# Kernel optimization log

Measured on AMD Instinct MI355X. Metric: run time of the kernel, lower is better.

## Reference

```python
import jax, jax.numpy as jnp
import numpy as np

H = W = 224  # output confidence map size


def setup_inputs() -> dict:
    key = jax.random.key(0)
    k_x, k_w1, k_b1, k_w2, k_b2 = jax.random.split(key, 5)
    N = 500_000  # number of detections in the clip
    x = jax.random.uniform(k_x, (N, 7), dtype=jnp.float32)
    W1 = jax.random.normal(k_w1, (7, 64), dtype=jnp.float32) * (1.0 / np.sqrt(7.0))
    b1 = jax.random.normal(k_b1, (64,), dtype=jnp.float32) * 0.01
    W2 = jax.random.normal(k_w2, (64, H * W), dtype=jnp.float32) * (1.0 / 8.0)
    b2 = jax.random.normal(k_b2, (H * W,), dtype=jnp.float32) * 0.01
    return {"x": x, "W1": W1, "b1": b1, "W2": W2, "b2": b2}


def reference(x, W1, b1, W2, b2):
    # Encoder branch of Track_Block.forward:
    # silu -> Linear(7,64) -> silu -> mean over detections -> Linear(64,224*224)
    # -> silu -> reshape(224,224) -> clamp(0,1)
    h = jax.nn.silu(x)                       # [N, 7]
    h = jax.nn.silu(h @ W1 + b1)             # [N, 64]
    m = jnp.mean(h, axis=0)                  # [64] (mean over detection dim)
    e = jax.nn.silu(m @ W2 + b2)             # [50176]
    return jnp.clip(e.reshape(H, W), 0.0, 1.0)
```

## Files before the change

kernel.cpp:

```cpp
#include <hip/hip_runtime.h>
#include <hip/hip_bf16.h>

#define HWOUT 50176
#define NBLK  1024
#define CHUNK 256

typedef __attribute__((ext_vector_type(8))) short short8;
typedef __attribute__((ext_vector_type(4))) float f32x4;

__device__ __forceinline__ float fast_sigmoid(float x) {
    float t = __builtin_amdgcn_exp2f(-1.44269504088896340736f * x);
    return __builtin_amdgcn_rcpf(1.0f + t);
}
__device__ __forceinline__ float silu_f(float x) { return x * fast_sigmoid(x); }

__device__ __forceinline__ short to_bf16_bits(float f) {
    unsigned u = __builtin_bit_cast(unsigned, f);
    u += 0x7FFFu + ((u >> 16) & 1u);
    return (short)(u >> 16);
}

__global__ __launch_bounds__(256) void k_stage1(const float* __restrict__ x,
                                                const float* __restrict__ W1,
                                                const float* __restrict__ b1,
                                                float* __restrict__ partial,
                                                int N) {
    __shared__ short xs[CHUNK * 8];
    __shared__ float red[4][64];
    const int t = threadIdx.x;
    const int lane = t & 63;
    const int wave = t >> 6;

    const int krow = (lane >> 4) * 8;
    const int c = lane & 15;
    short8 bf[4];
    float bcol[4];
#pragma unroll
    for (int g = 0; g < 4; ++g) {
#pragma unroll
        for (int j = 0; j < 8; ++j) {
            int k = krow + j;
            float v = (k < 7) ? W1[k * 64 + g * 16 + c] : 0.0f;
            bf[g][j] = to_bf16_bits(v);
        }
        bcol[g] = b1[g * 16 + c];
    }

    float accf[4] = {0.0f, 0.0f, 0.0f, 0.0f};
    const int nchunk = (N + CHUNK - 1) / CHUNK;
    const short8 zero8 = {0, 0, 0, 0, 0, 0, 0, 0};
    const f32x4 zero4 = {0.0f, 0.0f, 0.0f, 0.0f};

    for (int ch = blockIdx.x; ch < nchunk; ch += NBLK) {
        const int row = ch * CHUNK + t;
        __syncthreads();
        {
            float v[7];
            if (row < N) {
#pragma unroll
                for (int k = 0; k < 7; ++k) v[k] = x[row * 7 + k];
            } else {
#pragma unroll
                for (int k = 0; k < 7; ++k) v[k] = 0.0f;
            }
            short8 p;
#pragma unroll
            for (int k = 0; k < 7; ++k) p[k] = to_bf16_bits(silu_f(v[k]));
            p[7] = 0;
            *reinterpret_cast<short8*>(&xs[t * 8]) = p;
        }
        __syncthreads();

        const bool full = (ch * CHUNK + CHUNK <= N);
        const int chbase = ch * CHUNK;
#pragma unroll
        for (int tt = 0; tt < 4; ++tt) {
            const int tile = wave * 4 + tt;
            short8 av = *reinterpret_cast<short8*>(&xs[(tile * 16 + c) * 8]);
            av = (lane < 16) ? av : zero8;
#pragma unroll
            for (int g = 0; g < 4; ++g) {
                f32x4 d = __builtin_amdgcn_mfma_f32_16x16x32_bf16(av, bf[g], zero4, 0, 0, 0);
                if (full) {
#pragma unroll
                    for (int r = 0; r < 4; ++r) accf[g] += silu_f(d[r] + bcol[g]);
                } else {
                    const int r0 = chbase + tile * 16 + (lane >> 4) * 4;
#pragma unroll
                    for (int r = 0; r < 4; ++r) {
                        float s = silu_f(d[r] + bcol[g]);
                        accf[g] += (r0 + r < N) ? s : 0.0f;
                    }
                }
            }
        }
    }

#pragma unroll
    for (int g = 0; g < 4; ++g) {
        accf[g] += __shfl_xor(accf[g], 16, 64);
        accf[g] += __shfl_xor(accf[g], 32, 64);
    }
    if (lane < 16) {
#pragma unroll
        for (int g = 0; g < 4; ++g) red[wave][g * 16 + lane] = accf[g];
    }
    __syncthreads();
    if (t < 64)
        partial[blockIdx.x * 64 + t] = red[0][t] + red[1][t] + red[2][t] + red[3][t];
}

__global__ __launch_bounds__(256) void k_out2(const float* __restrict__ partial,
                                              const float* __restrict__ W2,
                                              const float* __restrict__ b2,
                                              float* __restrict__ out,
                                              float invN) {
    __shared__ float4 red[256];
    __shared__ float ml[64];
    const int t = threadIdx.x;
    const int c4 = t & 15;
    const int grp = t >> 4;
    const float4* p4 = reinterpret_cast<const float4*>(partial);

    float4 s = {0.0f, 0.0f, 0.0f, 0.0f};
#pragma unroll 8
    for (int r = grp; r < NBLK; r += 16) {
        float4 v = p4[r * 16 + c4];
        s.x += v.x; s.y += v.y; s.z += v.z; s.w += v.w;
    }
    red[t] = s;
    __syncthreads();
    if (t < 16) {
        float4 a = {0.0f, 0.0f, 0.0f, 0.0f};
#pragma unroll
        for (int g = 0; g < 16; ++g) {
            float4 v = red[g * 16 + t];
            a.x += v.x; a.y += v.y; a.z += v.z; a.w += v.w;
        }
        ml[4 * t + 0] = a.x * invN;
        ml[4 * t + 1] = a.y * invN;
        ml[4 * t + 2] = a.z * invN;
        ml[4 * t + 3] = a.w * invN;
    }
    __syncthreads();

    const int j = blockIdx.x * 256 + t;
    float acc = b2[j];
#pragma unroll
    for (int k4 = 0; k4 < 16; ++k4) {
        float4 mv = *reinterpret_cast<float4*>(&ml[k4 * 4]);
        acc = fmaf(mv.x, W2[(k4 * 4 + 0) * HWOUT + j], acc);
        acc = fmaf(mv.y, W2[(k4 * 4 + 1) * HWOUT + j], acc);
        acc = fmaf(mv.z, W2[(k4 * 4 + 2) * HWOUT + j], acc);
        acc = fmaf(mv.w, W2[(k4 * 4 + 3) * HWOUT + j], acc);
    }
    float e = silu_f(acc);
    out[j] = fminf(fmaxf(e, 0.0f), 1.0f);
}

extern "C" void kernel_launch(void* const* d_in, const int* in_sizes, int n_in,
                              void* d_out, int out_size, void* d_ws, size_t ws_size,
                              hipStream_t stream) {
    const float* x  = (const float*)d_in[0];
    const float* W1 = (const float*)d_in[1];
    const float* b1 = (const float*)d_in[2];
    const float* W2 = (const float*)d_in[3];
    const float* b2 = (const float*)d_in[4];
    float* out = (float*)d_out;

    const int N = in_sizes[0] / 7;
    float* partial = (float*)d_ws;

    k_stage1<<<NBLK, 256, 0, stream>>>(x, W1, b1, partial, N);
    k_out2<<<HWOUT / 256, 256, 0, stream>>>(partial, W2, b2, out, 1.0f / (float)N);
}
```

Before: 25.74 us.

## Fuse both stages into one persistent kernel with atomic grid barrier

Merges the MLP-mean stage and the output projection into a single kernel of 256 blocks of 1024 threads. After each block writes its partial sums, an atomic counter with a spin-wait acts as a grid-wide barrier, and every block then reduces all partials itself. Each block computes 196 outputs, splitting K across four thread groups. Rows are loaded two per thread with float2 reads, and larger chunks are used. This removes the second kernel launch and its gap, but adds a memset launch and a spin barrier that depends on all 256 blocks being resident at the same time.

```diff
diff --git a/kernel.cpp b/kernel.cpp
--- a/kernel.cpp
+++ b/kernel.cpp
@@ -1,9 +1,9 @@
 #include <hip/hip_runtime.h>
-#include <hip/hip_bf16.h>
 
 #define HWOUT 50176
-#define NBLK  1024
-#define CHUNK 256
+#define GRID  256
+#define CHUNK 2048
+#define OUTPB 196
 
 typedef __attribute__((ext_vector_type(8))) short short8;
 typedef __attribute__((ext_vector_type(4))) float f32x4;
@@ -20,21 +20,28 @@
     return (short)(u >> 16);
 }
 
-__global__ __launch_bounds__(256) void k_stage1(const float* __restrict__ x,
-                                                const float* __restrict__ W1,
-                                                const float* __restrict__ b1,
-                                                float* __restrict__ partial,
-                                                int N) {
+__global__ __launch_bounds__(1024, 4) void k_fused(
+        const float* __restrict__ x,  const float* __restrict__ W1,
+        const float* __restrict__ b1, const float* __restrict__ W2,
+        const float* __restrict__ b2, float* __restrict__ out,
+        float* __restrict__ ws, int N, float invN) {
     __shared__ short xs[CHUNK * 8];
-    __shared__ float red[4][64];
-    const int t = threadIdx.x;
+    __shared__ float red[16][64];
+    __shared__ float msh[64];
+    __shared__ float osum[4][256];
+
+    unsigned* ctr = (unsigned*)ws;
+    float* partial = ws + 64;
+
+    const int t    = threadIdx.x;
     const int lane = t & 63;
     const int wave = t >> 6;
+    const int b    = blockIdx.x;
 
     const int krow = (lane >> 4) * 8;
-    const int c = lane & 15;
+    const int c    = lane & 15;
     short8 bf[4];
-    float bcol[4];
+    float  bcol[4];
 #pragma unroll
     for (int g = 0; g < 4; ++g) {
 #pragma unroll
@@ -47,35 +54,43 @@
     }
 
     float accf[4] = {0.0f, 0.0f, 0.0f, 0.0f};
-    const int nchunk = (N + CHUNK - 1) / CHUNK;
+    const int nch = (N + CHUNK - 1) / CHUNK;
     const short8 zero8 = {0, 0, 0, 0, 0, 0, 0, 0};
-    const f32x4 zero4 = {0.0f, 0.0f, 0.0f, 0.0f};
+    const f32x4  zero4 = {0.0f, 0.0f, 0.0f, 0.0f};
 
-    for (int ch = blockIdx.x; ch < nchunk; ch += NBLK) {
-        const int row = ch * CHUNK + t;
+    for (int ch = b; ch < nch; ch += GRID) {
         __syncthreads();
         {
-            float v[7];
-            if (row < N) {
+            const int r0 = ch * CHUNK + 2 * t;
+            float v[14];
+            if (r0 + 1 < N) {
+                const float2* p = reinterpret_cast<const float2*>(x + (size_t)r0 * 7);
 #pragma unroll
-                for (int k = 0; k < 7; ++k) v[k] = x[row * 7 + k];
+                for (int i = 0; i < 7; ++i) { float2 q = p[i]; v[2*i] = q.x; v[2*i+1] = q.y; }
             } else {
+                const long total = (long)N * 7;
 #pragma unroll
-                for (int k = 0; k < 7; ++k) v[k] = 0.0f;
+                for (int i = 0; i < 14; ++i) {
+                    long idx = (long)r0 * 7 + i;
+                    v[i] = (idx < total) ? x[idx] : 0.0f;
+                }
             }
-            short8 p;
+            short8 p0, p1;
 #pragma unroll
-            for (int k = 0; k < 7; ++k) p[k] = to_bf16_bits(silu_f(v[k]));
-            p[7] = 0;
-            *reinterpret_cast<short8*>(&xs[t * 8]) = p;
+            for (int k = 0; k < 7; ++k) {
+                p0[k] = to_bf16_bits(silu_f(v[k]));
+                p1[k] = to_bf16_bits(silu_f(v[7 + k]));
+            }
+            p0[7] = 0; p1[7] = 0;
+            *reinterpret_cast<short8*>(&xs[(2 * t + 0) * 8]) = p0;
+            *reinterpret_cast<short8*>(&xs[(2 * t + 1) * 8]) = p1;
         }
         __syncthreads();
 
         const bool full = (ch * CHUNK + CHUNK <= N);
-        const int chbase = ch * CHUNK;
 #pragma unroll
-        for (int tt = 0; tt < 4; ++tt) {
-            const int tile = wave * 4 + tt;
+        for (int tt = 0; tt < 8; ++tt) {
+            const int tile = wave * 8 + tt;
             short8 av = *reinterpret_cast<short8*>(&xs[(tile * 16 + c) * 8]);
             av = (lane < 16) ? av : zero8;
 #pragma unroll
@@ -85,11 +100,11 @@
 #pragma unroll
                     for (int r = 0; r < 4; ++r) accf[g] += silu_f(d[r] + bcol[g]);
                 } else {
-                    const int r0 = chbase + tile * 16 + (lane >> 4) * 4;
+                    const int r0g = ch * CHUNK + tile * 16 + (lane >> 4) * 4;
 #pragma unroll
                     for (int r = 0; r < 4; ++r) {
                         float s = silu_f(d[r] + bcol[g]);
-                        accf[g] += (r0 + r < N) ? s : 0.0f;
+                        accf[g] += (r0g + r < N) ? s : 0.0f;
                     }
                 }
             }
@@ -101,61 +116,66 @@
         accf[g] += __shfl_xor(accf[g], 16, 64);
         accf[g] += __shfl_xor(accf[g], 32, 64);
     }
+    __syncthreads();
     if (lane < 16) {
 #pragma unroll
         for (int g = 0; g < 4; ++g) red[wave][g * 16 + lane] = accf[g];
     }
     __syncthreads();
-    if (t < 64)
-        partial[blockIdx.x * 64 + t] = red[0][t] + red[1][t] + red[2][t] + red[3][t];
-}
+    if (t < 64) {
+        float s = 0.0f;
+#pragma unroll
+        for (int wv = 0; wv < 16; ++wv) s += red[wv][t];
+        partial[b * 64 + t] = s;
+    }
 
-__global__ __launch_bounds__(256) void k_out2(const float* __restrict__ partial,
-                                              const float* __restrict__ W2,
-                                              const float* __restrict__ b2,
-                                              float* __restrict__ out,
-                                              float invN) {
-    __shared__ float4 red[256];
-    __shared__ float ml[64];
-    const int t = threadIdx.x;
-    const int c4 = t & 15;
-    const int grp = t >> 4;
-    const float4* p4 = reinterpret_cast<const float4*>(partial);
-
-    float4 s = {0.0f, 0.0f, 0.0f, 0.0f};
-#pragma unroll 8
-    for (int r = grp; r < NBLK; r += 16) {
-        float4 v = p4[r * 16 + c4];
-        s.x += v.x; s.y += v.y; s.z += v.z; s.w += v.w;
-    }
-    red[t] = s;
     __syncthreads();
-    if (t < 16) {
-        float4 a = {0.0f, 0.0f, 0.0f, 0.0f};
-#pragma unroll
-        for (int g = 0; g < 16; ++g) {
-            float4 v = red[g * 16 + t];
-            a.x += v.x; a.y += v.y; a.z += v.z; a.w += v.w;
+    if (t == 0) {
+        __threadfence();
+        atomicAdd(ctr, 1u);
+        while (__hip_atomic_load(ctr, __ATOMIC_RELAXED, __HIP_MEMORY_SCOPE_AGENT)
+               < (unsigned)gridDim.x) {
+            __builtin_amdgcn_s_sleep(4);
         }
-        ml[4 * t + 0] = a.x * invN;
-        ml[4 * t + 1] = a.y * invN;
-        ml[4 * t + 2] = a.z * invN;
-        ml[4 * t + 3] = a.w * invN;
+        __threadfence();
     }
     __syncthreads();
 
-    const int j = blockIdx.x * 256 + t;
-    float acc = b2[j];
+    {
+        const int cc = t & 63, seg = t >> 6;
+        float s = 0.0f;
+#pragma unroll 4
+        for (int r = seg; r < GRID; r += 16) s += partial[r * 64 + cc];
+        red[seg][cc] = s;
+    }
+    __syncthreads();
+    if (t < 64) {
+        float s = 0.0f;
 #pragma unroll
-    for (int k4 = 0; k4 < 16; ++k4) {
-        float4 mv = *reinterpret_cast<float4*>(&ml[k4 * 4]);
-        acc = fmaf(mv.x, W2[(k4 * 4 + 0) * HWOUT + j], acc);
-        acc = fmaf(mv.y, W2[(k4 * 4 + 1) * HWOUT + j], acc);
-        acc = fmaf(mv.z, W2[(k4 * 4 + 2) * HWOUT + j], acc);
-        acc = fmaf(mv.w, W2[(k4 * 4 + 3) * HWOUT + j], acc);
+        for (int sg = 0; sg < 16; ++sg) s += red[sg][t];
+        msh[t] = s * invN;
     }
-    float e = silu_f(acc);
-    out[j] = fminf(fmaxf(e, 0.0f), 1.0f);
+    __syncthreads();
+
+    {
+        const int s = t >> 8;
+        const int i = t & 255;
+        float acc = 0.0f;
+        if (i < OUTPB) {
+            const int j = b * OUTPB + i;
+#pragma unroll
+            for (int k = 0; k < 16; ++k)
+                acc = fmaf(msh[s * 16 + k], W2[(size_t)(s * 16 + k) * HWOUT + j], acc);
+        }
+        osum[s][i] = acc;
+    }
+    __syncthreads();
+    if (t < OUTPB) {
+        const int j = b * OUTPB + t;
+        float e = osum[0][t] + osum[1][t] + osum[2][t] + osum[3][t] + b2[j];
+        e = silu_f(e);
+        out[j] = fminf(fmaxf(e, 0.0f), 1.0f);
+    }
 }
 
 extern "C" void kernel_launch(void* const* d_in, const int* in_sizes, int n_in,
@@ -169,8 +189,8 @@
     float* out = (float*)d_out;
 
     const int N = in_sizes[0] / 7;
-    float* partial = (float*)d_ws;
 
-    k_stage1<<<NBLK, 256, 0, stream>>>(x, W1, b1, partial, N);
-    k_out2<<<HWOUT / 256, 256, 0, stream>>>(partial, W2, b2, out, 1.0f / (float)N);
+    hipMemsetAsync(d_ws, 0, 64 * sizeof(float), stream);
+    k_fused<<<GRID, 1024, 0, stream>>>(x, W1, b1, W2, b2, out,
+                                       (float*)d_ws, N, 1.0f / (float)N);
 }
```

New measurement: 40.55 us. 57.5% more time.

## Fold bias into MFMA, remove tail masking, enlarge stage-1 blocks

Applied to the files above, without the earlier changes.

Stage 1 now runs 256 blocks of 1024 threads with 1024-row chunks. The bias is folded into the MFMA accumulator input and SiLU is computed in vector form, which removes the per-row boundary check. Padded rows contribute silu(b1) each, so the block that processes the last chunk subtracts phantom*silu(b1) as a correction. Stage 2 sums 256 partials instead of 1024 and uses 8 independent accumulators in the W2 dot product for more ILP. The trade-offs are lower occupancy flexibility with 1024-thread blocks and a slight numerical change from the subtraction-based tail correction.

```diff
diff --git a/kernel.cpp b/kernel.cpp
--- a/kernel.cpp
+++ b/kernel.cpp
@@ -1,9 +1,9 @@
 #include <hip/hip_runtime.h>
-#include <hip/hip_bf16.h>
 
 #define HWOUT 50176
-#define NBLK  1024
-#define CHUNK 256
+#define NBLK  256
+#define CHUNK 1024
+#define NWAVE 16
 
 typedef __attribute__((ext_vector_type(8))) short short8;
 typedef __attribute__((ext_vector_type(4))) float f32x4;
@@ -20,13 +20,13 @@
     return (short)(u >> 16);
 }
 
-__global__ __launch_bounds__(256) void k_stage1(const float* __restrict__ x,
-                                                const float* __restrict__ W1,
-                                                const float* __restrict__ b1,
-                                                float* __restrict__ partial,
-                                                int N) {
+__global__ __launch_bounds__(1024) void k_stage1(const float* __restrict__ x,
+                                                 const float* __restrict__ W1,
+                                                 const float* __restrict__ b1,
+                                                 float* __restrict__ partial,
+                                                 int N) {
     __shared__ short xs[CHUNK * 8];
-    __shared__ float red[4][64];
+    __shared__ float red[NWAVE][64];
     const int t = threadIdx.x;
     const int lane = t & 63;
     const int wave = t >> 6;
@@ -34,7 +34,7 @@
     const int krow = (lane >> 4) * 8;
     const int c = lane & 15;
     short8 bf[4];
-    float bcol[4];
+    f32x4 biasC[4];
 #pragma unroll
     for (int g = 0; g < 4; ++g) {
 #pragma unroll
@@ -43,22 +43,30 @@
             float v = (k < 7) ? W1[k * 64 + g * 16 + c] : 0.0f;
             bf[g][j] = to_bf16_bits(v);
         }
-        bcol[g] = b1[g * 16 + c];
-    }
-
-    float accf[4] = {0.0f, 0.0f, 0.0f, 0.0f};
+        float bb = b1[g * 16 + c];
+        biasC[g] = (f32x4){bb, bb, bb, bb};
+    }
+
+    f32x4 accv[4];
+#pragma unroll
+    for (int g = 0; g < 4; ++g) accv[g] = (f32x4){0.0f, 0.0f, 0.0f, 0.0f};
+
     const int nchunk = (N + CHUNK - 1) / CHUNK;
     const short8 zero8 = {0, 0, 0, 0, 0, 0, 0, 0};
-    const f32x4 zero4 = {0.0f, 0.0f, 0.0f, 0.0f};
-
+    const f32x4 onev = {1.0f, 1.0f, 1.0f, 1.0f};
+    const f32x4 nlog2e = {-1.44269504088896f, -1.44269504088896f,
+                          -1.44269504088896f, -1.44269504088896f};
+
+    bool did_last = false;
     for (int ch = blockIdx.x; ch < nchunk; ch += NBLK) {
+        did_last |= (ch == nchunk - 1);
         const int row = ch * CHUNK + t;
         __syncthreads();
         {
             float v[7];
             if (row < N) {
 #pragma unroll
-                for (int k = 0; k < 7; ++k) v[k] = x[row * 7 + k];
+                for (int k = 0; k < 7; ++k) v[k] = x[(size_t)row * 7 + k];
             } else {
 #pragma unroll
                 for (int k = 0; k < 7; ++k) v[k] = 0.0f;
@@ -71,8 +79,6 @@
         }
         __syncthreads();
 
-        const bool full = (ch * CHUNK + CHUNK <= N);
-        const int chbase = ch * CHUNK;
 #pragma unroll
         for (int tt = 0; tt < 4; ++tt) {
             const int tile = wave * 4 + tt;
@@ -80,34 +86,47 @@
             av = (lane < 16) ? av : zero8;
 #pragma unroll
             for (int g = 0; g < 4; ++g) {
-                f32x4 d = __builtin_amdgcn_mfma_f32_16x16x32_bf16(av, bf[g], zero4, 0, 0, 0);
-                if (full) {
-#pragma unroll
-                    for (int r = 0; r < 4; ++r) accf[g] += silu_f(d[r] + bcol[g]);
-                } else {
-                    const int r0 = chbase + tile * 16 + (lane >> 4) * 4;
-#pragma unroll
-                    for (int r = 0; r < 4; ++r) {
-                        float s = silu_f(d[r] + bcol[g]);
-                        accf[g] += (r0 + r < N) ? s : 0.0f;
-                    }
-                }
+                f32x4 d = __builtin_amdgcn_mfma_f32_16x16x32_bf16(av, bf[g], biasC[g], 0, 0, 0);
+                f32x4 targ = d * nlog2e;
+                f32x4 ex;
+                ex[0] = __builtin_amdgcn_exp2f(targ[0]);
+                ex[1] = __builtin_amdgcn_exp2f(targ[1]);
+                ex[2] = __builtin_amdgcn_exp2f(targ[2]);
+                ex[3] = __builtin_amdgcn_exp2f(targ[3]);
+                f32x4 den = ex + onev;
+                f32x4 r;
+                r[0] = __builtin_amdgcn_rcpf(den[0]);
+                r[1] = __builtin_amdgcn_rcpf(den[1]);
+                r[2] = __builtin_amdgcn_rcpf(den[2]);
+                r[3] = __builtin_amdgcn_rcpf(den[3]);
+                accv[g] = d * r + accv[g];
             }
         }
     }
 
+    float accf[4];
 #pragma unroll
     for (int g = 0; g < 4; ++g) {
+        accf[g] = (accv[g][0] + accv[g][1]) + (accv[g][2] + accv[g][3]);
         accf[g] += __shfl_xor(accf[g], 16, 64);
         accf[g] += __shfl_xor(accf[g], 32, 64);
     }
+    __syncthreads();
     if (lane < 16) {
 #pragma unroll
         for (int g = 0; g < 4; ++g) red[wave][g * 16 + lane] = accf[g];
     }
     __syncthreads();
-    if (t < 64)
-        partial[blockIdx.x * 64 + t] = red[0][t] + red[1][t] + red[2][t] + red[3][t];
+    if (t < 64) {
+        float s = 0.0f;
+#pragma unroll
+        for (int wv = 0; wv < NWAVE; ++wv) s += red[wv][t];
+        if (did_last) {
+            const int phantom = nchunk * CHUNK - N;
+            s -= (float)phantom * silu_f(b1[t]);
+        }
+        partial[blockIdx.x * 64 + t] = s;
+    }
 }
 
 __global__ __launch_bounds__(256) void k_out2(const float* __restrict__ partial,
@@ -123,7 +142,7 @@
     const float4* p4 = reinterpret_cast<const float4*>(partial);
 
     float4 s = {0.0f, 0.0f, 0.0f, 0.0f};
-#pragma unroll 8
+#pragma unroll
     for (int r = grp; r < NBLK; r += 16) {
         float4 v = p4[r * 16 + c4];
         s.x += v.x; s.y += v.y; s.z += v.z; s.w += v.w;
@@ -145,16 +164,21 @@
     __syncthreads();
 
     const int j = blockIdx.x * 256 + t;
-    float acc = b2[j];
-#pragma unroll
-    for (int k4 = 0; k4 < 16; ++k4) {
-        float4 mv = *reinterpret_cast<float4*>(&ml[k4 * 4]);
-        acc = fmaf(mv.x, W2[(k4 * 4 + 0) * HWOUT + j], acc);
-        acc = fmaf(mv.y, W2[(k4 * 4 + 1) * HWOUT + j], acc);
-        acc = fmaf(mv.z, W2[(k4 * 4 + 2) * HWOUT + j], acc);
-        acc = fmaf(mv.w, W2[(k4 * 4 + 3) * HWOUT + j], acc);
-    }
-    float e = silu_f(acc);
+    float acc[8];
+#pragma unroll
+    for (int i = 0; i < 8; ++i) acc[i] = 0.0f;
+#pragma unroll
+    for (int k8 = 0; k8 < 8; ++k8) {
+#pragma unroll
+        for (int i = 0; i < 8; ++i) {
+            const int k = k8 * 8 + i;
+            acc[i] = fmaf(ml[k], W2[(size_t)k * HWOUT + j], acc[i]);
+        }
+    }
+    float a01 = acc[0] + acc[1], a23 = acc[2] + acc[3];
+    float a45 = acc[4] + acc[5], a67 = acc[6] + acc[7];
+    float e = ((a01 + a23) + (a45 + a67)) + b2[j];
+    e = silu_f(e);
     out[j] = fminf(fmaxf(e, 0.0f), 1.0f);
 }
 
@@ -171,6 +195,6 @@
     const int N = in_sizes[0] / 7;
     float* partial = (float*)d_ws;
 
-    k_stage1<<<NBLK, 256, 0, stream>>>(x, W1, b1, partial, N);
+    k_stage1<<<NBLK, 1024, 0, stream>>>(x, W1, b1, partial, N);
     k_out2<<<HWOUT / 256, 256, 0, stream>>>(partial, W2, b2, out, 1.0f / (float)N);
 }
```

After: 23.56 us. 1.09x faster.
